# Performance work log

Measured on AMD Instinct MI355X. Metric: run time of the kernel, lower is better.

The kernel has to match this reference:

```python
import jax, jax.numpy as jnp
import numpy as np

D_MODEL = 2048
H_Q = 32
H_KV = 8
D_HEAD = D_MODEL // H_Q  # 64
Q_PER_KV = H_Q // H_KV   # 4
B, L = 2, 2048


def setup_inputs() -> dict:
    key = jax.random.key(0)
    kx, kq, kk, kv, ko = jax.random.split(key, 5)
    s = 0.02
    return {
        "x": jax.random.normal(kx, (B, L, D_MODEL), dtype=jnp.float32),
        "Wq": jax.random.normal(kq, (D_MODEL, D_MODEL), dtype=jnp.float32) * s,
        "Wk": jax.random.normal(kk, (D_MODEL, D_HEAD * H_KV), dtype=jnp.float32) * s,
        "Wv": jax.random.normal(kv, (D_MODEL, D_HEAD * H_KV), dtype=jnp.float32) * s,
        "Wo": jax.random.normal(ko, (D_MODEL, D_MODEL), dtype=jnp.float32) * s,
    }


def reference(x, Wq, Wk, Wv, Wo):
    Bb, Ll, _ = x.shape
    # Projections (nn.Linear with bias=False -> x @ W; weights stored as (in, out))
    Q = (x @ Wq).reshape(Bb, Ll, H_Q, D_HEAD)          # (B, L, Hq, d)
    K = (x @ Wk).reshape(Bb, Ll, H_KV, D_HEAD)         # (B, L, Hkv, d)
    V = (x @ Wv).reshape(Bb, Ll, H_KV, D_HEAD)
    # Group query heads: (B, Hkv, q_per_kv, L, d)
    Q = Q.transpose(0, 2, 1, 3).reshape(Bb, H_KV, Q_PER_KV, Ll, D_HEAD)
    K = K.transpose(0, 2, 1, 3)                        # (B, Hkv, L, d)
    V = V.transpose(0, 2, 1, 3)
    scale = 1.0 / jnp.sqrt(jnp.asarray(D_HEAD, dtype=x.dtype))
    # scores: (B, Hkv, q_per_kv, L, L)
    scores = jnp.einsum('bhgqd,bhkd->bhgqk', Q, K) * scale
    attn = jax.nn.softmax(scores, axis=-1)
    out = jnp.einsum('bhgqk,bhkd->bhgqd', attn, V)     # (B, Hkv, g, L, d)
    out = out.reshape(Bb, H_Q, Ll, D_HEAD).transpose(0, 2, 1, 3).reshape(Bb, Ll, D_MODEL)
    return out @ Wo
```

## Files before the change

### kernel.cpp

```cpp
#include <hip/hip_runtime.h>
#include <hip/hip_bf16.h>
#include <cstdint>

#define D_MODEL 2048
#define HQ 32
#define HKV 8
#define DH 64
#define NB 2
#define LSEQ 2048
#define MROWS (NB*LSEQ)
#define KVB 64

typedef __attribute__((ext_vector_type(8))) short short8;
typedef __attribute__((ext_vector_type(4))) float f32x4;
typedef __attribute__((ext_vector_type(4))) unsigned short ushort4v;
typedef __attribute__((ext_vector_type(4))) unsigned int uint4v;
typedef unsigned short ushort;

__device__ __forceinline__ ushort f2bf(float f) {
    unsigned u = __float_as_uint(f);
    u += 0x7fffu + ((u >> 16) & 1u);
    return (ushort)(u >> 16);
}

__device__ __forceinline__ float ex2(float x) {
    float r;
    asm volatile("v_exp_f32 %0, %1\n\ts_nop 0" : "=v"(r) : "v"(x));
    return r;
}

__device__ __forceinline__ unsigned cvtpk(float a, float b) {
    unsigned r;
    asm("v_cvt_pk_bf16_f32 %0, %1, %2" : "=v"(r) : "v"(a), "v"(b));
    return r;
}

__device__ __forceinline__ void gload_lds16(const ushort* gsrc, ushort* ldst) {
    __builtin_amdgcn_global_load_lds((const __attribute__((address_space(1))) void*)gsrc,
                                     (__attribute__((address_space(3))) void*)ldst, 16, 0, 0);
}

__global__ __launch_bounds__(256)
void cvt_bf16_k(const float* __restrict__ in, ushort* __restrict__ out, int n4) {
    int i = blockIdx.x * blockDim.x + threadIdx.x;
    if (i < n4) {
        float4 v = *(const float4*)(in + (size_t)i * 4);
        ushort4v o = {f2bf(v.x), f2bf(v.y), f2bf(v.z), f2bf(v.w)};
        *(ushort4v*)(out + (size_t)i * 4) = o;
    }
}

__global__ __launch_bounds__(256)
void transpose_all(const float* __restrict__ Wq, const float* __restrict__ Wk,
                   const float* __restrict__ Wv, const float* __restrict__ Wo,
                   ushort* __restrict__ dst) {
    __shared__ float t[32][33];
    const int tid = threadIdx.x;
    const int n0 = blockIdx.x * 32, k0 = blockIdx.y * 32;
    const float* W; int Nd, nl;
    if (n0 < 2048)      { W = Wq; Nd = 2048; nl = n0; }
    else if (n0 < 2560) { W = Wk; Nd = 512;  nl = n0 - 2048; }
    else if (n0 < 3072) { W = Wv; Nd = 512;  nl = n0 - 2560; }
    else                { W = Wo; Nd = 2048; nl = n0 - 3072; }
    const int r = tid >> 3, c4 = (tid & 7) << 2;
    float4 v = *(const float4*)(W + (size_t)(k0 + r) * Nd + nl + c4);
    t[r][c4 + 0] = v.x; t[r][c4 + 1] = v.y; t[r][c4 + 2] = v.z; t[r][c4 + 3] = v.w;
    __syncthreads();
    const int n = tid >> 3, kc = (tid & 7) << 2;
    ushort4v o = {f2bf(t[kc + 0][n]), f2bf(t[kc + 1][n]), f2bf(t[kc + 2][n]), f2bf(t[kc + 3][n])};
    *(ushort4v*)(dst + (size_t)(n0 + n) * 2048 + k0 + kc) = o;
}

template<int BM, int MODE>
__global__ __launch_bounds__(256, 2)
void gemm_bf16(const ushort* __restrict__ A, const ushort* __restrict__ Bt,
               void* __restrict__ Cv, int M, int N, int K, float scale)
{
    constexpr int BN = 128;
    constexpr int FM = BM / 32;
    constexpr int ISSA = BM / 64;
    __shared__ __align__(16) ushort smem[2 * (BM + BN) * 32];
    ushort* As = smem;
    ushort* Bs = smem + 2 * BM * 32;

    const int tid = threadIdx.x;
    const int w = tid >> 6;
    const int wr = w >> 1, wc = w & 1;
    const int g = (tid & 63) >> 4, r16 = tid & 15;
    const int bm = blockIdx.y * BM, bn = blockIdx.x * BN;
    const int srow = tid >> 2, sphys = tid & 3;

    f32x4 acc[FM][4];
#pragma unroll
    for (int i = 0; i < FM; ++i)
#pragma unroll
        for (int j = 0; j < 4; ++j) acc[i][j] = {0.f, 0.f, 0.f, 0.f};

    auto stage = [&](int buf, int k0) {
#pragma unroll
        for (int i = 0; i < ISSA; ++i) {
            int row = i * 64 + srow;
            int slog = sphys ^ ((row >> 1) & 3);
            gload_lds16(A + (size_t)(bm + row) * K + k0 + slog * 8,
                        As + buf * BM * 32 + (i * 64 + w * 16) * 32);
        }
#pragma unroll
        for (int i = 0; i < 2; ++i) {
            int row = i * 64 + srow;
            int slog = sphys ^ ((row >> 1) & 3);
            gload_lds16(Bt + (size_t)(bn + row) * K + k0 + slog * 8,
                        Bs + buf * 128 * 32 + (i * 64 + w * 16) * 32);
        }
    };

    const int NTk = K >> 5;
    stage(0, 0);
    __syncthreads();
    int buf = 0;
    for (int kt = 0; kt < NTk; ++kt) {
        if (kt + 1 < NTk) stage(buf ^ 1, (kt + 1) << 5);
        const ushort* Ab = As + buf * BM * 32;
        const ushort* Bb = Bs + buf * 128 * 32;
        short8 af[FM], bfv[4];
#pragma unroll
        for (int mi = 0; mi < FM; ++mi) {
            int row = wr * (BM / 2) + mi * 16 + r16;
            int p = g ^ ((row >> 1) & 3);
            af[mi] = *(const short8*)(Ab + row * 32 + p * 8);
        }
#pragma unroll
        for (int ni = 0; ni < 4; ++ni) {
            int row = wc * 64 + ni * 16 + r16;
            int p = g ^ ((row >> 1) & 3);
            bfv[ni] = *(const short8*)(Bb + row * 32 + p * 8);
        }
#pragma unroll
        for (int mi = 0; mi < FM; ++mi)
#pragma unroll
            for (int ni = 0; ni < 4; ++ni)
                acc[mi][ni] = __builtin_amdgcn_mfma_f32_16x16x32_bf16(af[mi], bfv[ni], acc[mi][ni], 0, 0, 0);
        __syncthreads();
        buf ^= 1;
    }

    float* C = (float*)Cv;
#pragma unroll
    for (int mi = 0; mi < FM; ++mi)
#pragma unroll
        for (int ni = 0; ni < 4; ++ni)
#pragma unroll
            for (int r = 0; r < 4; ++r) {
                int row = bm + wr * (BM / 2) + mi * 16 + g * 4 + r;
                int col = bn + wc * 64 + ni * 16 + r16;
                C[(size_t)row * N + col] = acc[mi][ni][r] * scale;
            }
}

__global__ __launch_bounds__(256, 2)
void gemm_qkv(const ushort* __restrict__ A, const ushort* __restrict__ Bt,
              ushort* __restrict__ Qd, ushort* __restrict__ Kd, ushort* __restrict__ Vd,
              float qscale)
{
    constexpr int K = 2048;
    __shared__ __align__(16) ushort smem[2 * 256 * 32];

    const int tid = threadIdx.x;
    const int l = tid & 63;
    const int w = tid >> 6;
    const int wr = w >> 1, wc = w & 1;
    const int g = l >> 4, r16 = l & 15;
    const int bm = blockIdx.y * 128, bn = blockIdx.x * 128;
    const int srow = tid >> 2, sphys = tid & 3;

    ushort* As = smem;
    ushort* Bs = smem + 2 * 128 * 32;

    f32x4 acc[4][4];
#pragma unroll
    for (int i = 0; i < 4; ++i)
#pragma unroll
        for (int j = 0; j < 4; ++j) acc[i][j] = {0.f, 0.f, 0.f, 0.f};

    auto stage = [&](int buf, int k0) {
#pragma unroll
        for (int i = 0; i < 2; ++i) {
            int row = i * 64 + srow;
            int slog = sphys ^ ((row >> 1) & 3);
            gload_lds16(A + (size_t)(bm + row) * K + k0 + slog * 8,
                        As + buf * 128 * 32 + (i * 64 + w * 16) * 32);
            gload_lds16(Bt + (size_t)(bn + row) * K + k0 + slog * 8,
                        Bs + buf * 128 * 32 + (i * 64 + w * 16) * 32);
        }
    };

    stage(0, 0);
    __syncthreads();
    int buf = 0;
    for (int kt = 0; kt < K / 32; ++kt) {
        if (kt + 1 < K / 32) stage(buf ^ 1, (kt + 1) << 5);
        const ushort* Ab = As + buf * 128 * 32;
        const ushort* Bb = Bs + buf * 128 * 32;
        short8 af[4], bfv[4];
#pragma unroll
        for (int mi = 0; mi < 4; ++mi) {
            int row = wr * 64 + mi * 16 + r16;
            int p = g ^ ((row >> 1) & 3);
            af[mi] = *(const short8*)(Ab + row * 32 + p * 8);
        }
#pragma unroll
        for (int ni = 0; ni < 4; ++ni) {
            int row = wc * 64 + ni * 16 + r16;
            int p = g ^ ((row >> 1) & 3);
            bfv[ni] = *(const short8*)(Bb + row * 32 + p * 8);
        }
#pragma unroll
        for (int mi = 0; mi < 4; ++mi)
#pragma unroll
            for (int ni = 0; ni < 4; ++ni)
                acc[mi][ni] = __builtin_amdgcn_mfma_f32_16x16x32_bf16(af[mi], bfv[ni], acc[mi][ni], 0, 0, 0);
        __syncthreads();
        buf ^= 1;
    }

    const int colbase = bn + wc * 64;
    const int rowbase = bm + wr * 64;
    const int b = rowbase >> 11;
    const int l0 = rowbase & (LSEQ - 1);
    ushort* Ls = smem + w * 64 * 64;
    __syncthreads();

    if (colbase < 2560) {
        const float sc = (colbase < 2048) ? qscale : 1.f;
#pragma unroll
        for (int mi = 0; mi < 4; ++mi)
#pragma unroll
            for (int ni = 0; ni < 4; ++ni)
#pragma unroll
                for (int r = 0; r < 4; ++r)
                    Ls[(mi * 16 + g * 4 + r) * 64 + ni * 16 + r16] = f2bf(acc[mi][ni][r] * sc);
        __syncthreads();
        ushort* dst;
        if (colbase < 2048)
            dst = Qd + (((size_t)(b * 32 + (colbase >> 6))) * LSEQ + l0) * 64;
        else
            dst = Kd + (((size_t)(b * 8 + ((colbase - 2048) >> 6))) * LSEQ + l0) * 64;
#pragma unroll
        for (int c = 0; c < 8; ++c) {
            int idx = c * 64 + l;
            *(short8*)(dst + idx * 8) = *(const short8*)(Ls + idx * 8);
        }
    } else {
#pragma unroll
        for (int mi = 0; mi < 4; ++mi)
#pragma unroll
            for (int ni = 0; ni < 4; ++ni) {
                ushort4v pk = {f2bf(acc[mi][ni][0]), f2bf(acc[mi][ni][1]),
                               f2bf(acc[mi][ni][2]), f2bf(acc[mi][ni][3])};
                *(ushort4v*)(&Ls[(((mi >> 1) * 64 + ni * 16 + r16) * 4 + g) * 8 + (mi & 1) * 4]) = pk;
            }
        __syncthreads();
        const int h = (colbase - 2560) >> 6;
        ushort* dst = Vd + (((size_t)(b * 8 + h)) * 64 + (l0 >> 5)) * 2048;
#pragma unroll
        for (int c = 0; c < 8; ++c) {
            int idx = c * 64 + l;
            *(short8*)(dst + (size_t)idx * 8) = *(const short8*)(Ls + idx * 8);
        }
    }
}

__global__ __launch_bounds__(256, 2)
void attn_bf16(const ushort* __restrict__ Qb, const ushort* __restrict__ Kb,
               const ushort* __restrict__ Vtb, ushort* __restrict__ Ob)
{
    __shared__ __align__(16) ushort Ks[2][KVB * 64];
    __shared__ __align__(16) ushort Vs[2][KVB * 64];

    const int tid = threadIdx.x;
    const int l = tid & 63, w = tid >> 6;
    const int g = l >> 4, r16 = l & 15;
    const int bh = blockIdx.y, b = bh >> 5, hq = bh & 31, hk = hq >> 2;
    const int q0 = blockIdx.x * 128 + w * 32;

    const ushort* Qh = Qb + (size_t)bh * LSEQ * 64;
    const ushort* Kh = Kb + (size_t)(b * HKV + hk) * LSEQ * 64;
    const ushort* Vh = Vtb + (size_t)(b * HKV + hk) * 64 * LSEQ;

    short8 qf[2][2];
#pragma unroll
    for (int qb = 0; qb < 2; ++qb)
#pragma unroll
        for (int dh = 0; dh < 2; ++dh)
            qf[qb][dh] = *(const short8*)(Qh + (size_t)(q0 + qb * 16 + r16) * 64 + dh * 32 + g * 8);

    short8 ones;
#pragma unroll
    for (int j = 0; j < 8; ++j) ones[j] = (short)0x3F80;

    f32x4 acco[4][2];
#pragma unroll
    for (int i = 0; i < 4; ++i)
#pragma unroll
        for (int j = 0; j < 2; ++j) acco[i][j] = {0.f, 0.f, 0.f, 0.f};
    f32x4 accl[2] = {{0.f, 0.f, 0.f, 0.f}, {0.f, 0.f, 0.f, 0.f}};

    const int sr = tid >> 3, sp = tid & 7;

    auto stage = [&](ushort* kdst, ushort* vdst, int k0) {
        const int slog = sp ^ (sr & 7);
#pragma unroll
        for (int i = 0; i < 2; ++i)
            gload_lds16(Kh + (size_t)(k0 + i * 32 + sr) * 64 + slog * 8,
                        kdst + i * 2048 + w * 512);
#pragma unroll
        for (int i = 0; i < 2; ++i)
            gload_lds16(Vh + (size_t)k0 * 64 + i * 2048 + (size_t)tid * 8,
                        vdst + i * 2048 + w * 512);
    };

    auto body = [&](const ushort* Kc, const ushort* Vc, ushort* Kn, ushort* Vn, int t) {
        if (t + 1 < LSEQ / KVB) stage(Kn, Vn, (t + 1) * KVB);

        f32x4 sacc[4][2];
#pragma unroll
        for (int kb = 0; kb < 4; ++kb) {
            const int row = kb * 16 + r16, c = r16 & 7;
            short8 kf0 = *(const short8*)(Kc + row * 64 + ((g) ^ c) * 8);
            short8 kf1 = *(const short8*)(Kc + row * 64 + ((4 + g) ^ c) * 8);
#pragma unroll
            for (int qb = 0; qb < 2; ++qb) {
                f32x4 z = {0.f, 0.f, 0.f, 0.f};
                z = __builtin_amdgcn_mfma_f32_16x16x32_bf16(kf0, qf[qb][0], z, 0, 0, 0);
                sacc[kb][qb] = __builtin_amdgcn_mfma_f32_16x16x32_bf16(kf1, qf[qb][1], z, 0, 0, 0);
            }
        }

        short8 vf[4][2];
#pragma unroll
        for (int db = 0; db < 4; ++db)
#pragma unroll
            for (int s = 0; s < 2; ++s)
                vf[db][s] = *(const short8*)(Vc + ((s * 64 + db * 16 + r16) * 4 + g) * 8);

        short8 pf[2][2];
#pragma unroll
        for (int qb = 0; qb < 2; ++qb) {
            float p[16];
#pragma unroll
            for (int kb = 0; kb < 4; ++kb)
#pragma unroll
                for (int r = 0; r < 4; ++r)
                    p[kb * 4 + r] = ex2(sacc[kb][qb][r]);
#pragma unroll
            for (int s = 0; s < 2; ++s) {
                uint4v pu;
                pu[0] = cvtpk(p[s * 8 + 0], p[s * 8 + 1]);
                pu[1] = cvtpk(p[s * 8 + 2], p[s * 8 + 3]);
                pu[2] = cvtpk(p[s * 8 + 4], p[s * 8 + 5]);
                pu[3] = cvtpk(p[s * 8 + 6], p[s * 8 + 7]);
                pf[s][qb] = *(short8*)&pu;
            }
        }

#pragma unroll
        for (int db = 0; db < 4; ++db)
#pragma unroll
            for (int qb = 0; qb < 2; ++qb) {
                acco[db][qb] = __builtin_amdgcn_mfma_f32_16x16x32_bf16(vf[db][0], pf[0][qb], acco[db][qb], 0, 0, 0);
                acco[db][qb] = __builtin_amdgcn_mfma_f32_16x16x32_bf16(vf[db][1], pf[1][qb], acco[db][qb], 0, 0, 0);
            }
#pragma unroll
        for (int qb = 0; qb < 2; ++qb) {
            accl[qb] = __builtin_amdgcn_mfma_f32_16x16x32_bf16(ones, pf[0][qb], accl[qb], 0, 0, 0);
            accl[qb] = __builtin_amdgcn_mfma_f32_16x16x32_bf16(ones, pf[1][qb], accl[qb], 0, 0, 0);
        }

        __syncthreads();
    };

    stage(Ks[0], Vs[0], 0);
    __syncthreads();
    for (int kt = 0; kt < LSEQ / KVB; kt += 2) {
        body(Ks[0], Vs[0], Ks[1], Vs[1], kt);
        body(Ks[1], Vs[1], Ks[0], Vs[0], kt + 1);
    }

    float inv[2] = {1.f / accl[0][0], 1.f / accl[1][0]};
#pragma unroll
    for (int qb = 0; qb < 2; ++qb)
#pragma unroll
        for (int db = 0; db < 4; ++db) {
            int lseq = q0 + qb * 16 + r16;
            ushort4v o = {f2bf(acco[db][qb][0] * inv[qb]), f2bf(acco[db][qb][1] * inv[qb]),
                          f2bf(acco[db][qb][2] * inv[qb]), f2bf(acco[db][qb][3] * inv[qb])};
            *(ushort4v*)(Ob + ((size_t)b * LSEQ + lseq) * D_MODEL + hq * 64 + db * 16 + g * 4) = o;
        }
}

extern "C" void kernel_launch(void* const* d_in, const int* in_sizes, int n_in,
                              void* d_out, int out_size, void* d_ws, size_t ws_size,
                              hipStream_t stream)
{
    const float* x  = (const float*)d_in[0];
    const float* Wq = (const float*)d_in[1];
    const float* Wk = (const float*)d_in[2];
    const float* Wv = (const float*)d_in[3];
    const float* Wo = (const float*)d_in[4];

    ushort* xb  = (ushort*)d_ws;
    ushort* Ob  = xb;
    ushort* Wf  = xb  + (size_t)MROWS * D_MODEL;
    ushort* Wot = Wf  + (size_t)3072 * D_MODEL;
    ushort* Kbf = Wot + (size_t)D_MODEL * D_MODEL;
    ushort* Vtb = Kbf + (size_t)NB * HKV * LSEQ * DH;
    ushort* Qbf = (ushort*)d_out;

    dim3 blk(256);
    cvt_bf16_k<<<dim3((MROWS * D_MODEL / 4 + 255) / 256), blk, 0, stream>>>(x, xb, MROWS * D_MODEL / 4);
    transpose_all<<<dim3(5120 / 32, D_MODEL / 32), blk, 0, stream>>>(Wq, Wk, Wv, Wo, Wf);

    gemm_qkv<<<dim3(3072 / 128, MROWS / 128), blk, 0, stream>>>(
        xb, Wf, Qbf, Kbf, Vtb, 0.125f * 1.44269504f);

    attn_bf16<<<dim3(LSEQ / 128, NB * HQ), blk, 0, stream>>>(Qbf, Kbf, Vtb, Ob);

    gemm_bf16<128, 0><<<dim3(D_MODEL / 128, MROWS / 128), blk, 0, stream>>>(
        Ob, Wot, d_out, MROWS, D_MODEL, D_MODEL, 1.f);
}
```

Before: 192.8 us.

## Replace GEMMs with 512-thread 128x256 tile kernel using triple-buffered pipeline

Merges the QKV and output projection GEMMs into one templated kernel that runs 8 waves per block over a 128x256 tile. It moves from double to triple buffering, using explicit vmcnt waits and raw s_barrier so two tiles of loads stay in flight. It also raises MFMA priority with s_setprio. The larger tile improves operand reuse, but it uses more LDS per block and cuts the grid to fewer blocks, which may lower occupancy.

```diff
diff --git a/kernel.cpp b/kernel.cpp
--- a/kernel.cpp
+++ b/kernel.cpp
@@ -71,200 +71,133 @@
     *(ushort4v*)(dst + (size_t)(n0 + n) * 2048 + k0 + kc) = o;
 }
 
-template<int BM, int MODE>
-__global__ __launch_bounds__(256, 2)
-void gemm_bf16(const ushort* __restrict__ A, const ushort* __restrict__ Bt,
-               void* __restrict__ Cv, int M, int N, int K, float scale)
+template<int MODE>
+__global__ __launch_bounds__(512, 2)
+void gemm512(const ushort* __restrict__ A, const ushort* __restrict__ Bt,
+             float* __restrict__ Cf, ushort* __restrict__ Qd, ushort* __restrict__ Kd,
+             ushort* __restrict__ Vd, int N, int K, float qscale)
 {
-    constexpr int BN = 128;
-    constexpr int FM = BM / 32;
-    constexpr int ISSA = BM / 64;
-    __shared__ __align__(16) ushort smem[2 * (BM + BN) * 32];
-    ushort* As = smem;
-    ushort* Bs = smem + 2 * BM * 32;
-
+    __shared__ __align__(16) ushort smem[3 * 12288];
     const int tid = threadIdx.x;
-    const int w = tid >> 6;
-    const int wr = w >> 1, wc = w & 1;
-    const int g = (tid & 63) >> 4, r16 = tid & 15;
-    const int bm = blockIdx.y * BM, bn = blockIdx.x * BN;
+    const int l = tid & 63, w = tid >> 6;
+    const int wr = w >> 2, wc = w & 3;
+    const int g = l >> 4, r16 = l & 15;
+    const int bm = blockIdx.y * 128, bn = blockIdx.x * 256;
     const int srow = tid >> 2, sphys = tid & 3;
 
-    f32x4 acc[FM][4];
-#pragma unroll
-    for (int i = 0; i < FM; ++i)
+    f32x4 acc[4][4];
+#pragma unroll
+    for (int i = 0; i < 4; ++i)
 #pragma unroll
         for (int j = 0; j < 4; ++j) acc[i][j] = {0.f, 0.f, 0.f, 0.f};
 
-    auto stage = [&](int buf, int k0) {
-#pragma unroll
-        for (int i = 0; i < ISSA; ++i) {
-            int row = i * 64 + srow;
-            int slog = sphys ^ ((row >> 1) & 3);
-            gload_lds16(A + (size_t)(bm + row) * K + k0 + slog * 8,
-                        As + buf * BM * 32 + (i * 64 + w * 16) * 32);
+    auto stage = [&](ushort* buf, int t) {
+        const int k0 = t << 5;
+        {
+            int slog = sphys ^ ((srow >> 1) & 3);
+            gload_lds16(A + (size_t)(bm + srow) * K + k0 + slog * 8, buf + w * 512);
         }
 #pragma unroll
         for (int i = 0; i < 2; ++i) {
-            int row = i * 64 + srow;
+            int row = i * 128 + srow;
             int slog = sphys ^ ((row >> 1) & 3);
             gload_lds16(Bt + (size_t)(bn + row) * K + k0 + slog * 8,
-                        Bs + buf * 128 * 32 + (i * 64 + w * 16) * 32);
+                        buf + 4096 + i * 4096 + w * 512);
         }
     };
 
-    const int NTk = K >> 5;
-    stage(0, 0);
-    __syncthreads();
-    int buf = 0;
-    for (int kt = 0; kt < NTk; ++kt) {
-        if (kt + 1 < NTk) stage(buf ^ 1, (kt + 1) << 5);
-        const ushort* Ab = As + buf * BM * 32;
-        const ushort* Bb = Bs + buf * 128 * 32;
-        short8 af[FM], bfv[4];
-#pragma unroll
-        for (int mi = 0; mi < FM; ++mi) {
-            int row = wr * (BM / 2) + mi * 16 + r16;
-            int p = g ^ ((row >> 1) & 3);
-            af[mi] = *(const short8*)(Ab + row * 32 + p * 8);
-        }
-#pragma unroll
-        for (int ni = 0; ni < 4; ++ni) {
-            int row = wc * 64 + ni * 16 + r16;
-            int p = g ^ ((row >> 1) & 3);
-            bfv[ni] = *(const short8*)(Bb + row * 32 + p * 8);
-        }
-#pragma unroll
-        for (int mi = 0; mi < FM; ++mi)
+    ushort* b0 = smem;
+    ushort* b1 = smem + 12288;
+    ushort* b2 = smem + 24576;
+    stage(b0, 0);
+    stage(b1, 1);
+    asm volatile("s_waitcnt vmcnt(3)" ::: "memory");
+    __builtin_amdgcn_s_barrier();
+    __builtin_amdgcn_sched_barrier(0);
+
+    const int NT = K >> 5;
+    for (int t = 0; t < NT; ++t) {
+        if (t + 2 < NT) stage(b2, t + 2);
+        const ushort* Ab = b0;
+        const ushort* Bb = b0 + 4096;
+        short8 bf[4];
+#pragma unroll
+        for (int n = 0; n < 4; ++n) {
+            int row = wc * 64 + n * 16 + r16;
+            bf[n] = *(const short8*)(Bb + row * 32 + (g ^ ((row >> 1) & 3)) * 8);
+        }
+#pragma unroll
+        for (int m = 0; m < 4; ++m) {
+            int row = wr * 64 + m * 16 + r16;
+            short8 af = *(const short8*)(Ab + row * 32 + (g ^ ((row >> 1) & 3)) * 8);
+            __builtin_amdgcn_s_setprio(1);
+#pragma unroll
+            for (int n = 0; n < 4; ++n)
+                acc[m][n] = __builtin_amdgcn_mfma_f32_16x16x32_bf16(af, bf[n], acc[m][n], 0, 0, 0);
+            __builtin_amdgcn_s_setprio(0);
+        }
+        if (t + 2 < NT) asm volatile("s_waitcnt vmcnt(3)" ::: "memory");
+        else            asm volatile("s_waitcnt vmcnt(0)" ::: "memory");
+        __builtin_amdgcn_s_barrier();
+        __builtin_amdgcn_sched_barrier(0);
+        ushort* tp = b0; b0 = b1; b1 = b2; b2 = tp;
+    }
+
+    if (MODE == 0) {
+#pragma unroll
+        for (int mi = 0; mi < 4; ++mi)
 #pragma unroll
             for (int ni = 0; ni < 4; ++ni)
-                acc[mi][ni] = __builtin_amdgcn_mfma_f32_16x16x32_bf16(af[mi], bfv[ni], acc[mi][ni], 0, 0, 0);
+#pragma unroll
+                for (int r = 0; r < 4; ++r) {
+                    int row = bm + wr * 64 + mi * 16 + g * 4 + r;
+                    int col = bn + wc * 64 + ni * 16 + r16;
+                    Cf[(size_t)row * N + col] = acc[mi][ni][r];
+                }
+    } else {
+        const int colbase = bn + wc * 64;
+        const int rowbase = bm + wr * 64;
+        const int b = rowbase >> 11;
+        const int l0 = rowbase & (LSEQ - 1);
+        ushort* Ls = smem + w * 4096;
         __syncthreads();
-        buf ^= 1;
-    }
-
-    float* C = (float*)Cv;
-#pragma unroll
-    for (int mi = 0; mi < FM; ++mi)
-#pragma unroll
-        for (int ni = 0; ni < 4; ++ni)
-#pragma unroll
-            for (int r = 0; r < 4; ++r) {
-                int row = bm + wr * (BM / 2) + mi * 16 + g * 4 + r;
-                int col = bn + wc * 64 + ni * 16 + r16;
-                C[(size_t)row * N + col] = acc[mi][ni][r] * scale;
-            }
-}
-
-__global__ __launch_bounds__(256, 2)
-void gemm_qkv(const ushort* __restrict__ A, const ushort* __restrict__ Bt,
-              ushort* __restrict__ Qd, ushort* __restrict__ Kd, ushort* __restrict__ Vd,
-              float qscale)
-{
-    constexpr int K = 2048;
-    __shared__ __align__(16) ushort smem[2 * 256 * 32];
-
-    const int tid = threadIdx.x;
-    const int l = tid & 63;
-    const int w = tid >> 6;
-    const int wr = w >> 1, wc = w & 1;
-    const int g = l >> 4, r16 = l & 15;
-    const int bm = blockIdx.y * 128, bn = blockIdx.x * 128;
-    const int srow = tid >> 2, sphys = tid & 3;
-
-    ushort* As = smem;
-    ushort* Bs = smem + 2 * 128 * 32;
-
-    f32x4 acc[4][4];
-#pragma unroll
-    for (int i = 0; i < 4; ++i)
-#pragma unroll
-        for (int j = 0; j < 4; ++j) acc[i][j] = {0.f, 0.f, 0.f, 0.f};
-
-    auto stage = [&](int buf, int k0) {
-#pragma unroll
-        for (int i = 0; i < 2; ++i) {
-            int row = i * 64 + srow;
-            int slog = sphys ^ ((row >> 1) & 3);
-            gload_lds16(A + (size_t)(bm + row) * K + k0 + slog * 8,
-                        As + buf * 128 * 32 + (i * 64 + w * 16) * 32);
-            gload_lds16(Bt + (size_t)(bn + row) * K + k0 + slog * 8,
-                        Bs + buf * 128 * 32 + (i * 64 + w * 16) * 32);
-        }
-    };
-
-    stage(0, 0);
-    __syncthreads();
-    int buf = 0;
-    for (int kt = 0; kt < K / 32; ++kt) {
-        if (kt + 1 < K / 32) stage(buf ^ 1, (kt + 1) << 5);
-        const ushort* Ab = As + buf * 128 * 32;
-        const ushort* Bb = Bs + buf * 128 * 32;
-        short8 af[4], bfv[4];
-#pragma unroll
-        for (int mi = 0; mi < 4; ++mi) {
-            int row = wr * 64 + mi * 16 + r16;
-            int p = g ^ ((row >> 1) & 3);
-            af[mi] = *(const short8*)(Ab + row * 32 + p * 8);
-        }
-#pragma unroll
-        for (int ni = 0; ni < 4; ++ni) {
-            int row = wc * 64 + ni * 16 + r16;
-            int p = g ^ ((row >> 1) & 3);
-            bfv[ni] = *(const short8*)(Bb + row * 32 + p * 8);
-        }
-#pragma unroll
-        for (int mi = 0; mi < 4; ++mi)
-#pragma unroll
-            for (int ni = 0; ni < 4; ++ni)
-                acc[mi][ni] = __builtin_amdgcn_mfma_f32_16x16x32_bf16(af[mi], bfv[ni], acc[mi][ni], 0, 0, 0);
-        __syncthreads();
-        buf ^= 1;
-    }
-
-    const int colbase = bn + wc * 64;
-    const int rowbase = bm + wr * 64;
-    const int b = rowbase >> 11;
-    const int l0 = rowbase & (LSEQ - 1);
-    ushort* Ls = smem + w * 64 * 64;
-    __syncthreads();
-
-    if (colbase < 2560) {
-        const float sc = (colbase < 2048) ? qscale : 1.f;
-#pragma unroll
-        for (int mi = 0; mi < 4; ++mi)
-#pragma unroll
-            for (int ni = 0; ni < 4; ++ni)
-#pragma unroll
-                for (int r = 0; r < 4; ++r)
-                    Ls[(mi * 16 + g * 4 + r) * 64 + ni * 16 + r16] = f2bf(acc[mi][ni][r] * sc);
-        __syncthreads();
-        ushort* dst;
-        if (colbase < 2048)
-            dst = Qd + (((size_t)(b * 32 + (colbase >> 6))) * LSEQ + l0) * 64;
-        else
-            dst = Kd + (((size_t)(b * 8 + ((colbase - 2048) >> 6))) * LSEQ + l0) * 64;
-#pragma unroll
-        for (int c = 0; c < 8; ++c) {
-            int idx = c * 64 + l;
-            *(short8*)(dst + idx * 8) = *(const short8*)(Ls + idx * 8);
-        }
-    } else {
-#pragma unroll
-        for (int mi = 0; mi < 4; ++mi)
-#pragma unroll
-            for (int ni = 0; ni < 4; ++ni) {
-                ushort4v pk = {f2bf(acc[mi][ni][0]), f2bf(acc[mi][ni][1]),
-                               f2bf(acc[mi][ni][2]), f2bf(acc[mi][ni][3])};
-                *(ushort4v*)(&Ls[(((mi >> 1) * 64 + ni * 16 + r16) * 4 + g) * 8 + (mi & 1) * 4]) = pk;
-            }
-        __syncthreads();
-        const int h = (colbase - 2560) >> 6;
-        ushort* dst = Vd + (((size_t)(b * 8 + h)) * 64 + (l0 >> 5)) * 2048;
-#pragma unroll
-        for (int c = 0; c < 8; ++c) {
-            int idx = c * 64 + l;
-            *(short8*)(dst + (size_t)idx * 8) = *(const short8*)(Ls + idx * 8);
+        if (colbase < 2560) {
+            const float sc = (colbase < 2048) ? qscale : 1.f;
+#pragma unroll
+            for (int mi = 0; mi < 4; ++mi)
+#pragma unroll
+                for (int ni = 0; ni < 4; ++ni)
+#pragma unroll
+                    for (int r = 0; r < 4; ++r)
+                        Ls[(mi * 16 + g * 4 + r) * 64 + ni * 16 + r16] = f2bf(acc[mi][ni][r] * sc);
+            __syncthreads();
+            ushort* dst;
+            if (colbase < 2048)
+                dst = Qd + (((size_t)(b * 32 + (colbase >> 6))) * LSEQ + l0) * 64;
+            else
+                dst = Kd + (((size_t)(b * 8 + ((colbase - 2048) >> 6))) * LSEQ + l0) * 64;
+#pragma unroll
+            for (int c = 0; c < 8; ++c) {
+                int idx = c * 64 + l;
+                *(short8*)(dst + idx * 8) = *(const short8*)(Ls + idx * 8);
+            }
+        } else {
+#pragma unroll
+            for (int mi = 0; mi < 4; ++mi)
+#pragma unroll
+                for (int ni = 0; ni < 4; ++ni) {
+                    ushort4v pk = {f2bf(acc[mi][ni][0]), f2bf(acc[mi][ni][1]),
+                                   f2bf(acc[mi][ni][2]), f2bf(acc[mi][ni][3])};
+                    *(ushort4v*)(&Ls[(((mi >> 1) * 64 + ni * 16 + r16) * 4 + g) * 8 + (mi & 1) * 4]) = pk;
+                }
+            __syncthreads();
+            const int h = (colbase - 2560) >> 6;
+            ushort* dst = Vd + (((size_t)(b * 8 + h)) * 64 + (l0 >> 5)) * 2048;
+#pragma unroll
+            for (int c = 0; c < 8; ++c) {
+                int idx = c * 64 + l;
+                *(short8*)(dst + (size_t)idx * 8) = *(const short8*)(Ls + idx * 8);
+            }
         }
     }
 }
@@ -419,11 +352,11 @@
     cvt_bf16_k<<<dim3((MROWS * D_MODEL / 4 + 255) / 256), blk, 0, stream>>>(x, xb, MROWS * D_MODEL / 4);
     transpose_all<<<dim3(5120 / 32, D_MODEL / 32), blk, 0, stream>>>(Wq, Wk, Wv, Wo, Wf);
 
-    gemm_qkv<<<dim3(3072 / 128, MROWS / 128), blk, 0, stream>>>(
-        xb, Wf, Qbf, Kbf, Vtb, 0.125f * 1.44269504f);
+    gemm512<1><<<dim3(3072 / 256, MROWS / 128), dim3(512), 0, stream>>>(
+        xb, Wf, nullptr, Qbf, Kbf, Vtb, 3072, 2048, 0.125f * 1.44269504f);
 
     attn_bf16<<<dim3(LSEQ / 128, NB * HQ), blk, 0, stream>>>(Qbf, Kbf, Vtb, Ob);
 
-    gemm_bf16<128, 0><<<dim3(D_MODEL / 128, MROWS / 128), blk, 0, stream>>>(
-        Ob, Wot, d_out, MROWS, D_MODEL, D_MODEL, 1.f);
-}
+    gemm512<0><<<dim3(D_MODEL / 256, MROWS / 128), dim3(512), 0, stream>>>(
+        Ob, Wot, (float*)d_out, nullptr, nullptr, nullptr, D_MODEL, 2048, 1.f);
+}
```

New measurement: 196.0 us. No clear change (+1.6%).

## Double per-warp query rows in attention and fuse exp into QK loop

Applied to the files above, without the earlier changes.

Each warp now handles 64 query rows instead of 32, so each block covers 256 queries and the grid halves. Every K/V tile loaded into LDS is reused across twice as many query rows, and each K/V fragment read from LDS feeds twice as many MFMAs. The exp2 and bf16 packing move right after each score MFMA, which removes the separate score buffer, and the inline asm exp is swapped for the compiler builtin. This raises register pressure (acco grows to 16 f32x4 under launch_bounds(256,2)) and leaves only 512 blocks, which may hurt occupancy or cause spills.

```diff
diff --git a/kernel.cpp b/kernel.cpp
--- a/kernel.cpp
+++ b/kernel.cpp
@@ -1,6 +1,7 @@
 #include <hip/hip_runtime.h>
 #include <hip/hip_bf16.h>
 #include <cstdint>
+#include <cmath>
 
 #define D_MODEL 2048
 #define HQ 32
@@ -17,21 +18,21 @@
 typedef __attribute__((ext_vector_type(4))) unsigned int uint4v;
 typedef unsigned short ushort;
 
+#if __has_builtin(__builtin_amdgcn_exp2f)
+#define EXP2(x) __builtin_amdgcn_exp2f(x)
+#else
+#define EXP2(x) exp2f(x)
+#endif
+
 __device__ __forceinline__ ushort f2bf(float f) {
     unsigned u = __float_as_uint(f);
     u += 0x7fffu + ((u >> 16) & 1u);
     return (ushort)(u >> 16);
 }
 
-__device__ __forceinline__ float ex2(float x) {
-    float r;
-    asm volatile("v_exp_f32 %0, %1\n\ts_nop 0" : "=v"(r) : "v"(x));
-    return r;
-}
-
-__device__ __forceinline__ unsigned cvtpk(float a, float b) {
+__device__ __forceinline__ unsigned cvtpk_sp(float a, float b) {
     unsigned r;
-    asm("v_cvt_pk_bf16_f32 %0, %1, %2" : "=v"(r) : "v"(a), "v"(b));
+    asm("s_nop 1\n\tv_cvt_pk_bf16_f32 %0, %1, %2" : "=v"(r) : "v"(a), "v"(b));
     return r;
 }
 
@@ -280,15 +281,15 @@
     const int l = tid & 63, w = tid >> 6;
     const int g = l >> 4, r16 = l & 15;
     const int bh = blockIdx.y, b = bh >> 5, hq = bh & 31, hk = hq >> 2;
-    const int q0 = blockIdx.x * 128 + w * 32;
+    const int q0 = blockIdx.x * 256 + w * 64;
 
     const ushort* Qh = Qb + (size_t)bh * LSEQ * 64;
     const ushort* Kh = Kb + (size_t)(b * HKV + hk) * LSEQ * 64;
     const ushort* Vh = Vtb + (size_t)(b * HKV + hk) * 64 * LSEQ;
 
-    short8 qf[2][2];
-#pragma unroll
-    for (int qb = 0; qb < 2; ++qb)
+    short8 qf[4][2];
+#pragma unroll
+    for (int qb = 0; qb < 4; ++qb)
 #pragma unroll
         for (int dh = 0; dh < 2; ++dh)
             qf[qb][dh] = *(const short8*)(Qh + (size_t)(q0 + qb * 16 + r16) * 64 + dh * 32 + g * 8);
@@ -297,12 +298,12 @@
 #pragma unroll
     for (int j = 0; j < 8; ++j) ones[j] = (short)0x3F80;
 
-    f32x4 acco[4][2];
+    f32x4 acco[4][4];
 #pragma unroll
     for (int i = 0; i < 4; ++i)
 #pragma unroll
-        for (int j = 0; j < 2; ++j) acco[i][j] = {0.f, 0.f, 0.f, 0.f};
-    f32x4 accl[2] = {{0.f, 0.f, 0.f, 0.f}, {0.f, 0.f, 0.f, 0.f}};
+        for (int j = 0; j < 4; ++j) acco[i][j] = {0.f, 0.f, 0.f, 0.f};
+    f32x4 accl[4] = {{0,0,0,0},{0,0,0,0},{0,0,0,0},{0,0,0,0}};
 
     const int sr = tid >> 3, sp = tid & 7;
 
@@ -321,17 +322,21 @@
     auto body = [&](const ushort* Kc, const ushort* Vc, ushort* Kn, ushort* Vn, int t) {
         if (t + 1 < LSEQ / KVB) stage(Kn, Vn, (t + 1) * KVB);
 
-        f32x4 sacc[4][2];
+        uint4v pw[2][4];
 #pragma unroll
         for (int kb = 0; kb < 4; ++kb) {
             const int row = kb * 16 + r16, c = r16 & 7;
             short8 kf0 = *(const short8*)(Kc + row * 64 + ((g) ^ c) * 8);
             short8 kf1 = *(const short8*)(Kc + row * 64 + ((4 + g) ^ c) * 8);
 #pragma unroll
-            for (int qb = 0; qb < 2; ++qb) {
+            for (int qb = 0; qb < 4; ++qb) {
                 f32x4 z = {0.f, 0.f, 0.f, 0.f};
                 z = __builtin_amdgcn_mfma_f32_16x16x32_bf16(kf0, qf[qb][0], z, 0, 0, 0);
-                sacc[kb][qb] = __builtin_amdgcn_mfma_f32_16x16x32_bf16(kf1, qf[qb][1], z, 0, 0, 0);
+                f32x4 sq = __builtin_amdgcn_mfma_f32_16x16x32_bf16(kf1, qf[qb][1], z, 0, 0, 0);
+                float p0 = EXP2(sq[0]), p1 = EXP2(sq[1]);
+                float p2 = EXP2(sq[2]), p3 = EXP2(sq[3]);
+                pw[kb >> 1][qb][(kb & 1) * 2 + 0] = cvtpk_sp(p0, p1);
+                pw[kb >> 1][qb][(kb & 1) * 2 + 1] = cvtpk_sp(p2, p3);
             }
         }
 
@@ -342,37 +347,21 @@
             for (int s = 0; s < 2; ++s)
                 vf[db][s] = *(const short8*)(Vc + ((s * 64 + db * 16 + r16) * 4 + g) * 8);
 
-        short8 pf[2][2];
-#pragma unroll
-        for (int qb = 0; qb < 2; ++qb) {
-            float p[16];
-#pragma unroll
-            for (int kb = 0; kb < 4; ++kb)
-#pragma unroll
-                for (int r = 0; r < 4; ++r)
-                    p[kb * 4 + r] = ex2(sacc[kb][qb][r]);
-#pragma unroll
-            for (int s = 0; s < 2; ++s) {
-                uint4v pu;
-                pu[0] = cvtpk(p[s * 8 + 0], p[s * 8 + 1]);
-                pu[1] = cvtpk(p[s * 8 + 2], p[s * 8 + 3]);
-                pu[2] = cvtpk(p[s * 8 + 4], p[s * 8 + 5]);
-                pu[3] = cvtpk(p[s * 8 + 6], p[s * 8 + 7]);
-                pf[s][qb] = *(short8*)&pu;
+#pragma unroll
+        for (int db = 0; db < 4; ++db)
+#pragma unroll
+            for (int qb = 0; qb < 4; ++qb) {
+                acco[db][qb] = __builtin_amdgcn_mfma_f32_16x16x32_bf16(
+                    vf[db][0], *(short8*)&pw[0][qb], acco[db][qb], 0, 0, 0);
+                acco[db][qb] = __builtin_amdgcn_mfma_f32_16x16x32_bf16(
+                    vf[db][1], *(short8*)&pw[1][qb], acco[db][qb], 0, 0, 0);
             }
-        }
-
-#pragma unroll
-        for (int db = 0; db < 4; ++db)
-#pragma unroll
-            for (int qb = 0; qb < 2; ++qb) {
-                acco[db][qb] = __builtin_amdgcn_mfma_f32_16x16x32_bf16(vf[db][0], pf[0][qb], acco[db][qb], 0, 0, 0);
-                acco[db][qb] = __builtin_amdgcn_mfma_f32_16x16x32_bf16(vf[db][1], pf[1][qb], acco[db][qb], 0, 0, 0);
-            }
-#pragma unroll
-        for (int qb = 0; qb < 2; ++qb) {
-            accl[qb] = __builtin_amdgcn_mfma_f32_16x16x32_bf16(ones, pf[0][qb], accl[qb], 0, 0, 0);
-            accl[qb] = __builtin_amdgcn_mfma_f32_16x16x32_bf16(ones, pf[1][qb], accl[qb], 0, 0, 0);
+#pragma unroll
+        for (int qb = 0; qb < 4; ++qb) {
+            accl[qb] = __builtin_amdgcn_mfma_f32_16x16x32_bf16(
+                ones, *(short8*)&pw[0][qb], accl[qb], 0, 0, 0);
+            accl[qb] = __builtin_amdgcn_mfma_f32_16x16x32_bf16(
+                ones, *(short8*)&pw[1][qb], accl[qb], 0, 0, 0);
         }
 
         __syncthreads();
@@ -385,9 +374,9 @@
         body(Ks[1], Vs[1], Ks[0], Vs[0], kt + 1);
     }
 
-    float inv[2] = {1.f / accl[0][0], 1.f / accl[1][0]};
-#pragma unroll
-    for (int qb = 0; qb < 2; ++qb)
+    float inv[4] = {1.f / accl[0][0], 1.f / accl[1][0], 1.f / accl[2][0], 1.f / accl[3][0]};
+#pragma unroll
+    for (int qb = 0; qb < 4; ++qb)
 #pragma unroll
         for (int db = 0; db < 4; ++db) {
             int lseq = q0 + qb * 16 + r16;
@@ -422,7 +411,7 @@
     gemm_qkv<<<dim3(3072 / 128, MROWS / 128), blk, 0, stream>>>(
         xb, Wf, Qbf, Kbf, Vtb, 0.125f * 1.44269504f);
 
-    attn_bf16<<<dim3(LSEQ / 128, NB * HQ), blk, 0, stream>>>(Qbf, Kbf, Vtb, Ob);
+    attn_bf16<<<dim3(LSEQ / 256, NB * HQ), blk, 0, stream>>>(Qbf, Kbf, Vtb, Ob);
 
     gemm_bf16<128, 0><<<dim3(D_MODEL / 128, MROWS / 128), blk, 0, stream>>>(
         Ob, Wot, d_out, MROWS, D_MODEL, D_MODEL, 1.f);
```

Result: no change. 191.9 us (-0.5%).
